# Performance work log

Measured on AMD Instinct MI355X. Metric: run time of the kernel, lower is better.

Reference implementation:

```python
import jax, jax.numpy as jnp
import numpy as np

B, N, H2, FD, P = 8, 128, 800, 500, 100


def setup_inputs() -> dict:
    key = jax.random.key(0)
    ks = jax.random.split(key, 20)
    w = lambda k, shape, s=0.05: jax.random.normal(k, shape, dtype=jnp.float32) * s
    return {
        "hidden_out": jax.random.normal(ks[0], (B, N, H2), dtype=jnp.float32),
        "Wh": w(ks[1], (FD, H2)), "bh": w(ks[2], (FD,)),
        "Wm": w(ks[3], (FD, H2)), "bm": w(ks[4], (FD,)),
        "Ws": w(ks[5], (FD, H2)), "bs": w(ks[6], (FD,)),
        "Wg": w(ks[7], (FD, H2)), "bg": w(ks[8], (FD,)),
        "W_gp": w(ks[9], (P, 3 * FD)), "b_gp": w(ks[10], (P,)),
        "W_sp": w(ks[11], (P, 3 * FD)), "b_sp": w(ks[12], (P,)),
        "W_rp": w(ks[13], (P, 2 * FD)), "b_rp": w(ks[14], (P,)),
        "w_go": w(ks[15], (1, P)), "b_go": w(ks[16], (1,)),
        "w_so": w(ks[17], (1, P)), "b_so": w(ks[18], (1,)),
    }


def reference(hidden_out, Wh, bh, Wm, bm, Ws, bs, Wg, bg,
              W_gp, b_gp, W_sp, b_sp, W_rp, b_rp,
              w_go, b_go, w_so, b_so):
    # hidden_out: [B, n, 2H]. Scores indexed [b, i(modifier), k(grand/sib), j(head)].
    n = hidden_out.shape[1]
    Fd = Wh.shape[0]
    # tanh(cat(...)) is elementwise, so tanh each per-position projection.
    head = jnp.tanh(jnp.einsum('bnh,fh->bnf', hidden_out, Wh) + bh)
    mod  = jnp.tanh(jnp.einsum('bnh,fh->bnf', hidden_out, Wm) + bm)
    sib  = jnp.tanh(jnp.einsum('bnh,fh->bnf', hidden_out, Ws) + bs)
    grd  = jnp.tanh(jnp.einsum('bnh,fh->bnf', hidden_out, Wg) + bg)

    # grand_out(grand_preout(x)) is a composed linear map (no nonlinearity between),
    # so the score decomposes into per-position scalars.
    vg, vgh, vgm = [(w_go @ W_gp[:, a * Fd:(a + 1) * Fd]).ravel() for a in range(3)]
    c_g = (b_gp @ w_go.ravel()) + b_go[0]
    gk = grd @ vg   # [B, n] grand position k
    gj = head @ vgh  # [B, n] head position j
    gi = mod @ vgm   # [B, n] modifier position i
    grand_val = jnp.tanh(gi[:, :, None, None] + gk[:, None, :, None]
                         + gj[:, None, None, :] + c_g)  # [B, i, k, j]

    vsh, vss, vsm = [(w_so @ W_sp[:, a * Fd:(a + 1) * Fd]).ravel() for a in range(3)]
    c_s = (b_sp @ w_so.ravel()) + b_so[0]
    sk = head @ vsh  # s-head at position k
    sj = sib @ vss   # sibling at position j
    si = mod @ vsm   # s-modifier at position i
    sib_val = jnp.tanh(si[:, :, None, None] + sk[:, None, :, None]
                       + sj[:, None, None, :] + c_s)

    idx = jnp.arange(n)
    i_ = idx[:, None, None]
    k_ = idx[None, :, None]
    j_ = idx[None, None, :]
    valid = (i_ != 0) & (i_ != j_) & (j_ != k_)  # main triple-index branch

    grand_scores = jnp.where(valid, grand_val, -jnp.inf)
    sibling_scores = jnp.where(valid, sib_val, jnp.float32(0.0))

    # root branch: j = k = 0, i != 0; uses root_preout then grand_out.
    r0 = head[:, 0] @ (w_go @ W_rp[:, :Fd]).ravel()        # [B]
    ri = mod @ (w_go @ W_rp[:, Fd:]).ravel()                # [B, n]
    root = jnp.tanh(r0[:, None] + ri + (b_rp @ w_go.ravel()) + b_go[0])
    grand_scores = grand_scores.at[:, 1:, 0, 0].set(root[:, 1:])

    return grand_scores, sibling_scores
```

## Files before the change

### kernel.cpp

```cpp
#include <hip/hip_runtime.h>
#include <math.h>

#define FD 500
#define H2 800
#define NB 8
#define NN 128
#define NR (NB*NN)
#define NC (4*FD)

#define NEG_HUGE (-1.0e30f)

__device__ __forceinline__ float fast_tanh(float x) {
    float e = __expf(2.0f * x);
    return 1.0f - 2.0f / (e + 1.0f);
}

__global__ void prep_kernel(const float* __restrict__ W_gp, const float* __restrict__ b_gp,
                            const float* __restrict__ W_sp, const float* __restrict__ b_sp,
                            const float* __restrict__ W_rp, const float* __restrict__ b_rp,
                            const float* __restrict__ w_go, const float* __restrict__ b_go,
                            const float* __restrict__ w_so, const float* __restrict__ b_so,
                            float* __restrict__ sel, float* __restrict__ consts) {
    int v = blockIdx.x;
    int f = threadIdx.x;
    const float* wvec; const float* mat; int cols; int off;
    if (v < 3)      { wvec = w_go; mat = W_gp; cols = 3*FD; off = v*FD; }
    else if (v < 6) { wvec = w_so; mat = W_sp; cols = 3*FD; off = (v-3)*FD; }
    else            { wvec = w_go; mat = W_rp; cols = 2*FD; off = (v-6)*FD; }
    if (f < FD) {
        float s = 0.f;
        #pragma unroll 4
        for (int p = 0; p < 100; ++p) s += wvec[p] * mat[p*cols + off + f];
        sel[v*512 + f] = s;
    }
    if (v == 0 && f >= FD && f < FD+3) {
        int which = f - FD;
        const float* bv; const float* wv; float badd;
        if (which == 0)      { bv = b_gp; wv = w_go; badd = b_go[0]; }
        else if (which == 1) { bv = b_sp; wv = w_so; badd = b_so[0]; }
        else                 { bv = b_rp; wv = w_go; badd = b_go[0]; }
        float s = badd;
        for (int p = 0; p < 100; ++p) s += bv[p] * wv[p];
        consts[which] = s;
    }
}

#define BM 64
#define BN 64
#define KT 16

__global__ __launch_bounds__(256) void gemm_tanh_kernel(
        const float* __restrict__ A,
        const float* __restrict__ Wh, const float* __restrict__ bh,
        const float* __restrict__ Wm, const float* __restrict__ bm,
        const float* __restrict__ Ws, const float* __restrict__ bs,
        const float* __restrict__ Wg, const float* __restrict__ bg,
        float* __restrict__ T) {
    __shared__ float As[KT][BM];
    __shared__ float Bs[KT][BN];
    int tid = threadIdx.x;
    int c0 = blockIdx.x * BN;
    int r0 = blockIdx.y * BM;

    int lm = tid & 63;
    int lk = tid >> 6;

    const float* arow = A + (size_t)(r0 + lm) * H2;

    int c = c0 + lm; if (c >= NC) c = NC - 1;
    int wt = c / FD, wf = c % FD;
    const float* wmat = (wt==0)?Wh:(wt==1)?Wm:(wt==2)?Ws:Wg;
    const float* wrow = wmat + (size_t)wf * H2;

    float acc[4][4];
    #pragma unroll
    for (int i=0;i<4;++i)
        #pragma unroll
        for (int j=0;j<4;++j) acc[i][j]=0.f;

    int tm = tid & 15;
    int tn = tid >> 4;

    float4 aReg = *(const float4*)(arow + lk*4);
    float4 wReg = *(const float4*)(wrow + lk*4);

    const int NT = H2 / KT;
    for (int kt = 0; kt < NT; ++kt) {
        __syncthreads();
        As[lk*4+0][lm] = aReg.x; As[lk*4+1][lm] = aReg.y;
        As[lk*4+2][lm] = aReg.z; As[lk*4+3][lm] = aReg.w;
        Bs[lk*4+0][lm] = wReg.x; Bs[lk*4+1][lm] = wReg.y;
        Bs[lk*4+2][lm] = wReg.z; Bs[lk*4+3][lm] = wReg.w;
        __syncthreads();
        if (kt+1 < NT) {
            aReg = *(const float4*)(arow + (kt+1)*KT + lk*4);
            wReg = *(const float4*)(wrow + (kt+1)*KT + lk*4);
        }
        #pragma unroll
        for (int k = 0; k < KT; ++k) {
            float4 a4 = *(const float4*)&As[k][tm*4];
            float4 b4 = *(const float4*)&Bs[k][tn*4];
            float av[4] = {a4.x,a4.y,a4.z,a4.w};
            float bv[4] = {b4.x,b4.y,b4.z,b4.w};
            #pragma unroll
            for (int i=0;i<4;++i)
                #pragma unroll
                for (int j=0;j<4;++j)
                    acc[i][j] += av[i]*bv[j];
        }
    }

    int cbase = c0 + tn*4;
    if (cbase < NC) {
        float bias[4];
        #pragma unroll
        for (int j=0;j<4;++j) {
            int cc = cbase + j;
            int t2 = cc / FD, f2 = cc % FD;
            const float* bb = (t2==0)?bh:(t2==1)?bm:(t2==2)?bs:bg;
            bias[j] = bb[f2];
        }
        #pragma unroll
        for (int i=0;i<4;++i) {
            int r = r0 + tm*4 + i;
            float4 o;
            o.x = fast_tanh(acc[i][0] + bias[0]);
            o.y = fast_tanh(acc[i][1] + bias[1]);
            o.z = fast_tanh(acc[i][2] + bias[2]);
            o.w = fast_tanh(acc[i][3] + bias[3]);
            *(float4*)(T + (size_t)r*NC + cbase) = o;
        }
    }
}

__global__ __launch_bounds__(256) void reduce_kernel(
        const float* __restrict__ T, const float* __restrict__ sel,
        float* __restrict__ rowvals) {
    int r = blockIdx.x;
    int tid = threadIdx.x;
    float p[8];
    #pragma unroll
    for (int q=0;q<8;++q) p[q]=0.f;
    const float* trow = T + (size_t)r * NC;
    for (int c = tid; c < NC; c += 256) {
        float y = trow[c];
        int t2 = c / FD, f2 = c % FD;
        if (t2 == 0) {
            p[1] += y * sel[1*512 + f2];
            p[5] += y * sel[3*512 + f2];
            p[7] += y * sel[6*512 + f2];
        } else if (t2 == 1) {
            p[0] += y * sel[2*512 + f2];
            p[3] += y * sel[5*512 + f2];
            p[6] += y * sel[7*512 + f2];
        } else if (t2 == 2) {
            p[4] += y * sel[4*512 + f2];
        } else {
            p[2] += y * sel[0*512 + f2];
        }
    }
    __shared__ float red[256][8];
    #pragma unroll
    for (int q=0;q<8;++q) red[tid][q] = p[q];
    __syncthreads();
    for (int s = 128; s > 0; s >>= 1) {
        if (tid < s) {
            #pragma unroll
            for (int q=0;q<8;++q) red[tid][q] += red[tid+s][q];
        }
        __syncthreads();
    }
    if (tid < 8) rowvals[(size_t)r*8 + tid] = red[0][tid];
}

#define KSPLIT 2
__global__ __launch_bounds__(256) void fill_kernel(
        const float* __restrict__ rowvals, const float* __restrict__ consts,
        float* __restrict__ grand, float* __restrict__ sib) {
    int bi = blockIdx.x;
    int kz = blockIdx.y;
    int b = bi >> 7;
    int i = bi & 127;
    int tid = threadIdx.x;

    __shared__ float gks[128], gjs[128], sks[128], sjs[128];
    if (tid < 128) {
        const float* rv = rowvals + (size_t)(b*128 + tid)*8;
        gks[tid] = rv[2];
        gjs[tid] = rv[1];
        sks[tid] = rv[5];
        sjs[tid] = rv[4];
    }
    __syncthreads();

    const float* rvi = rowvals + (size_t)bi * 8;
    float gi = rvi[0], si = rvi[3];
    float c_g = consts[0], c_s = consts[1], c_r = consts[2];
    float r0 = rowvals[(size_t)(b*128)*8 + 7];
    float ri = rvi[6];
    float rootv = fast_tanh(r0 + ri + c_r);

    size_t base = (size_t)bi * (128*128);

    int j4 = (tid & 31) * 4;
    int klo = tid >> 5;
    const int KROWS = 128 / KSPLIT;

    for (int it = 0; it < KROWS/8; ++it) {
        int k = kz*KROWS + it*8 + klo;
        float gk = gks[k], sk = sks[k];
        float4 go, so;
        #pragma unroll
        for (int jj = 0; jj < 4; ++jj) {
            int j = j4 + jj;
            bool valid = (i != 0) && (i != j) && (j != k);
            float g = valid ? fast_tanh(gi + gk + gjs[j] + c_g) : NEG_HUGE;
            float s = valid ? fast_tanh(si + sk + sjs[j] + c_s) : 0.0f;
            if (i != 0 && k == 0 && j == 0) g = rootv;
            (&go.x)[jj] = g;
            (&so.x)[jj] = s;
        }
        size_t off = base + (size_t)k*128 + j4;
        *(float4*)(grand + off) = go;
        *(float4*)(sib + off) = so;
    }
}

extern "C" void kernel_launch(void* const* d_in, const int* in_sizes, int n_in,
                              void* d_out, int out_size, void* d_ws, size_t ws_size,
                              hipStream_t stream) {
    const float* hidden = (const float*)d_in[0];
    const float* Wh  = (const float*)d_in[1];   const float* bh  = (const float*)d_in[2];
    const float* Wm  = (const float*)d_in[3];   const float* bm  = (const float*)d_in[4];
    const float* Ws_ = (const float*)d_in[5];   const float* bs  = (const float*)d_in[6];
    const float* Wg  = (const float*)d_in[7];   const float* bg  = (const float*)d_in[8];
    const float* W_gp = (const float*)d_in[9];  const float* b_gp = (const float*)d_in[10];
    const float* W_sp = (const float*)d_in[11]; const float* b_sp = (const float*)d_in[12];
    const float* W_rp = (const float*)d_in[13]; const float* b_rp = (const float*)d_in[14];
    const float* w_go = (const float*)d_in[15]; const float* b_go = (const float*)d_in[16];
    const float* w_so = (const float*)d_in[17]; const float* b_so = (const float*)d_in[18];

    float* out   = (float*)d_out;
    float* grand = out;
    float* sib   = out + (size_t)16777216;

    float* T       = (float*)d_ws;
    float* sel     = T + 2048000;
    float* consts  = sel + 4096;
    float* rowvals = consts + 16;

    prep_kernel<<<dim3(8), dim3(512), 0, stream>>>(W_gp, b_gp, W_sp, b_sp, W_rp, b_rp,
                                                   w_go, b_go, w_so, b_so, sel, consts);
    gemm_tanh_kernel<<<dim3(32,16), dim3(256), 0, stream>>>(hidden, Wh, bh, Wm, bm,
                                                            Ws_, bs, Wg, bg, T);
    reduce_kernel<<<dim3(NR), dim3(256), 0, stream>>>(T, sel, rowvals);
    fill_kernel<<<dim3(NR, KSPLIT), dim3(256), 0, stream>>>(rowvals, consts, grand, sib);
}
```

Baseline: 101.0 us.

## Use split-bf16 MFMA GEMM with fused tanh and projection reduction

Replaces the FP32 SIMT GEMM with a bf16x3 (hi/lo split) MFMA GEMM whose operands are pre-converted into a fragment-friendly tiled layout, staged through the output buffer as scratch. The tanh and the per-row dot products against the selector vectors are fused into the GEMM epilogue, which writes per-column-block partials instead of the full 1024x2000 activation matrix. A small finish kernel sums the partials. This removes the large intermediate write/read and the slow FP32 FMA loop, at the cost of extra convert passes and a small loss of precision from the split-bf16 emulation.

```diff
diff --git a/kernel.cpp b/kernel.cpp
--- a/kernel.cpp
+++ b/kernel.cpp
@@ -3,17 +3,23 @@
 
 #define FD 500
 #define H2 800
-#define NB 8
-#define NN 128
-#define NR (NB*NN)
-#define NC (4*FD)
+#define NRR 1024
+#define NPAD 2048
+#define NKS 25
 
 #define NEG_HUGE (-1.0e30f)
+
+typedef __bf16 bf16x8 __attribute__((ext_vector_type(8)));
+typedef float f32x4 __attribute__((ext_vector_type(4)));
+
+union ChunkU { uint4 u; bf16x8 b; __bf16 h[8]; };
 
 __device__ __forceinline__ float fast_tanh(float x) {
     float e = __expf(2.0f * x);
     return 1.0f - 2.0f / (e + 1.0f);
 }
+
+__device__ __forceinline__ bf16x8 as_frag(uint4 v) { ChunkU c; c.u = v; return c.b; }
 
 __global__ void prep_kernel(const float* __restrict__ W_gp, const float* __restrict__ b_gp,
                             const float* __restrict__ W_sp, const float* __restrict__ b_sp,
@@ -45,132 +51,176 @@
     }
 }
 
-#define BM 64
-#define BN 64
-#define KT 16
-
-__global__ __launch_bounds__(256) void gemm_tanh_kernel(
-        const float* __restrict__ A,
-        const float* __restrict__ Wh, const float* __restrict__ bh,
-        const float* __restrict__ Wm, const float* __restrict__ bm,
-        const float* __restrict__ Ws, const float* __restrict__ bs,
-        const float* __restrict__ Wg, const float* __restrict__ bg,
-        float* __restrict__ T) {
-    __shared__ float As[KT][BM];
-    __shared__ float Bs[KT][BN];
+__global__ void prep2_kernel(const float* __restrict__ sel,
+                             const float* __restrict__ bh, const float* __restrict__ bm,
+                             const float* __restrict__ bs, const float* __restrict__ bg,
+                             float* __restrict__ S8, float* __restrict__ bias_c) {
+    int c = blockIdx.x * 256 + threadIdx.x;
+    float v[8] = {0,0,0,0,0,0,0,0};
+    float bias = 0.f;
+    if (c < 2000) {
+        int t = c / FD, f = c % FD;
+        if (t == 0)      { v[1]=sel[1*512+f]; v[5]=sel[3*512+f]; v[7]=sel[6*512+f]; bias=bh[f]; }
+        else if (t == 1) { v[0]=sel[2*512+f]; v[3]=sel[5*512+f]; v[6]=sel[7*512+f]; bias=bm[f]; }
+        else if (t == 2) { v[4]=sel[4*512+f]; bias=bs[f]; }
+        else             { v[2]=sel[0*512+f]; bias=bg[f]; }
+    }
+    #pragma unroll
+    for (int q = 0; q < 8; ++q) S8[q*NPAD + c] = v[q];
+    bias_c[c] = bias;
+}
+
+__global__ __launch_bounds__(256) void convert_kernel(
+        const float* __restrict__ hidden,
+        const float* __restrict__ Wh, const float* __restrict__ Wm,
+        const float* __restrict__ Ws, const float* __restrict__ Wg,
+        uint4* __restrict__ A_t, uint4* __restrict__ B_t) {
+    int gid = blockIdx.x * 256 + threadIdx.x;
+    const float* src = nullptr;
+    uint4* dst;
+    int l, f;
+    if (gid < 102400) {
+        l = gid & 63; f = (gid >> 6) & 3;
+        int rest = gid >> 8;
+        int ks = rest % NKS, rb = rest / NKS;
+        int row = rb*64 + f*16 + (l & 15);
+        int k0 = ks*32 + (l >> 4)*8;
+        src = hidden + (size_t)row * H2 + k0;
+        dst = A_t + (size_t)(rb*NKS + ks) * 512;
+    } else {
+        int g2 = gid - 102400;
+        l = g2 & 63; f = (g2 >> 6) & 3;
+        int rest = g2 >> 8;
+        int ks = rest % NKS, cb = rest / NKS;
+        int c = cb*64 + f*16 + (l & 15);
+        int k0 = ks*32 + (l >> 4)*8;
+        if (c < 2000) {
+            int wt = c / FD, wf = c % FD;
+            const float* wm = (wt==0)?Wh:(wt==1)?Wm:(wt==2)?Ws:Wg;
+            src = wm + (size_t)wf * H2 + k0;
+        }
+        dst = B_t + (size_t)(cb*NKS + ks) * 512;
+    }
+    float x[8] = {0,0,0,0,0,0,0,0};
+    if (src) {
+        float4 v0 = *(const float4*)src;
+        float4 v1 = *(const float4*)(src + 4);
+        x[0]=v0.x; x[1]=v0.y; x[2]=v0.z; x[3]=v0.w;
+        x[4]=v1.x; x[5]=v1.y; x[6]=v1.z; x[7]=v1.w;
+    }
+    ChunkU hc, lo;
+    #pragma unroll
+    for (int j = 0; j < 8; ++j) {
+        __bf16 h = (__bf16)x[j];
+        hc.h[j] = h;
+        lo.h[j] = (__bf16)(x[j] - (float)h);
+    }
+    dst[(0*4 + f)*64 + l] = hc.u;
+    dst[(1*4 + f)*64 + l] = lo.u;
+}
+
+__global__ __launch_bounds__(256, 2) void gemm_kernel(
+        const uint4* __restrict__ A_t, const uint4* __restrict__ B_t,
+        const float* __restrict__ S8, const float* __restrict__ bias_c,
+        float* __restrict__ partials) {
+    __shared__ uint4 Abuf[2][512];
+    __shared__ uint4 Bbuf[2][512];
     int tid = threadIdx.x;
-    int c0 = blockIdx.x * BN;
-    int r0 = blockIdx.y * BM;
-
-    int lm = tid & 63;
-    int lk = tid >> 6;
-
-    const float* arow = A + (size_t)(r0 + lm) * H2;
-
-    int c = c0 + lm; if (c >= NC) c = NC - 1;
-    int wt = c / FD, wf = c % FD;
-    const float* wmat = (wt==0)?Wh:(wt==1)?Wm:(wt==2)?Ws:Wg;
-    const float* wrow = wmat + (size_t)wf * H2;
-
-    float acc[4][4];
-    #pragma unroll
-    for (int i=0;i<4;++i)
-        #pragma unroll
-        for (int j=0;j<4;++j) acc[i][j]=0.f;
-
-    int tm = tid & 15;
-    int tn = tid >> 4;
-
-    float4 aReg = *(const float4*)(arow + lk*4);
-    float4 wReg = *(const float4*)(wrow + lk*4);
-
-    const int NT = H2 / KT;
-    for (int kt = 0; kt < NT; ++kt) {
-        __syncthreads();
-        As[lk*4+0][lm] = aReg.x; As[lk*4+1][lm] = aReg.y;
-        As[lk*4+2][lm] = aReg.z; As[lk*4+3][lm] = aReg.w;
-        Bs[lk*4+0][lm] = wReg.x; Bs[lk*4+1][lm] = wReg.y;
-        Bs[lk*4+2][lm] = wReg.z; Bs[lk*4+3][lm] = wReg.w;
-        __syncthreads();
-        if (kt+1 < NT) {
-            aReg = *(const float4*)(arow + (kt+1)*KT + lk*4);
-            wReg = *(const float4*)(wrow + (kt+1)*KT + lk*4);
-        }
-        #pragma unroll
-        for (int k = 0; k < KT; ++k) {
-            float4 a4 = *(const float4*)&As[k][tm*4];
-            float4 b4 = *(const float4*)&Bs[k][tn*4];
-            float av[4] = {a4.x,a4.y,a4.z,a4.w};
-            float bv[4] = {b4.x,b4.y,b4.z,b4.w};
+    int cb = blockIdx.x;
+    int rb = blockIdx.y;
+    int l  = tid & 63;
+    int wid = tid >> 6;
+    int wr = wid >> 1, wc = wid & 1;
+
+    const uint4* Ablk = A_t + (size_t)rb * NKS * 512;
+    const uint4* Bblk = B_t + (size_t)cb * NKS * 512;
+
+    uint4 st[4];
+    #define STAGE_LOAD(ks) do { \
+        const uint4* s_ = (tid < 128) ? (Ablk + (ks)*512 + tid) : (Bblk + (ks)*512 + (tid-128)); \
+        st[0]=s_[0]; st[1]=s_[128]; st[2]=s_[256]; st[3]=s_[384]; } while(0)
+    #define STAGE_WRITE(buf) do { \
+        uint4* d_ = (tid < 128) ? &Abuf[buf][tid] : &Bbuf[buf][tid-128]; \
+        d_[0]=st[0]; d_[128]=st[1]; d_[256]=st[2]; d_[384]=st[3]; } while(0)
+
+    f32x4 acc[2][2];
+    #pragma unroll
+    for (int m=0;m<2;++m)
+        #pragma unroll
+        for (int n=0;n<2;++n) acc[m][n] = (f32x4){0.f,0.f,0.f,0.f};
+
+    STAGE_LOAD(0); STAGE_WRITE(0);
+    __syncthreads();
+    STAGE_LOAD(1);
+
+    for (int ks = 0; ks < NKS; ++ks) {
+        int cur = ks & 1;
+        int fa = wr*2, fb = wc*2;
+        bf16x8 a_h[2], a_l[2], b_h[2], b_l[2];
+        #pragma unroll
+        for (int m=0;m<2;++m) {
+            a_h[m] = as_frag(Abuf[cur][(0 + fa + m)*64 + l]);
+            a_l[m] = as_frag(Abuf[cur][(4 + fa + m)*64 + l]);
+        }
+        #pragma unroll
+        for (int n=0;n<2;++n) {
+            b_h[n] = as_frag(Bbuf[cur][(0 + fb + n)*64 + l]);
+            b_l[n] = as_frag(Bbuf[cur][(4 + fb + n)*64 + l]);
+        }
+        #pragma unroll
+        for (int m=0;m<2;++m)
             #pragma unroll
-            for (int i=0;i<4;++i)
-                #pragma unroll
-                for (int j=0;j<4;++j)
-                    acc[i][j] += av[i]*bv[j];
-        }
-    }
-
-    int cbase = c0 + tn*4;
-    if (cbase < NC) {
-        float bias[4];
-        #pragma unroll
-        for (int j=0;j<4;++j) {
-            int cc = cbase + j;
-            int t2 = cc / FD, f2 = cc % FD;
-            const float* bb = (t2==0)?bh:(t2==1)?bm:(t2==2)?bs:bg;
-            bias[j] = bb[f2];
-        }
-        #pragma unroll
-        for (int i=0;i<4;++i) {
-            int r = r0 + tm*4 + i;
-            float4 o;
-            o.x = fast_tanh(acc[i][0] + bias[0]);
-            o.y = fast_tanh(acc[i][1] + bias[1]);
-            o.z = fast_tanh(acc[i][2] + bias[2]);
-            o.w = fast_tanh(acc[i][3] + bias[3]);
-            *(float4*)(T + (size_t)r*NC + cbase) = o;
-        }
-    }
-}
-
-__global__ __launch_bounds__(256) void reduce_kernel(
-        const float* __restrict__ T, const float* __restrict__ sel,
-        float* __restrict__ rowvals) {
-    int r = blockIdx.x;
-    int tid = threadIdx.x;
-    float p[8];
-    #pragma unroll
-    for (int q=0;q<8;++q) p[q]=0.f;
-    const float* trow = T + (size_t)r * NC;
-    for (int c = tid; c < NC; c += 256) {
-        float y = trow[c];
-        int t2 = c / FD, f2 = c % FD;
-        if (t2 == 0) {
-            p[1] += y * sel[1*512 + f2];
-            p[5] += y * sel[3*512 + f2];
-            p[7] += y * sel[6*512 + f2];
-        } else if (t2 == 1) {
-            p[0] += y * sel[2*512 + f2];
-            p[3] += y * sel[5*512 + f2];
-            p[6] += y * sel[7*512 + f2];
-        } else if (t2 == 2) {
-            p[4] += y * sel[4*512 + f2];
-        } else {
-            p[2] += y * sel[0*512 + f2];
-        }
-    }
-    __shared__ float red[256][8];
-    #pragma unroll
-    for (int q=0;q<8;++q) red[tid][q] = p[q];
+            for (int n=0;n<2;++n) {
+                acc[m][n] = __builtin_amdgcn_mfma_f32_16x16x32_bf16(a_h[m], b_h[n], acc[m][n], 0,0,0);
+                acc[m][n] = __builtin_amdgcn_mfma_f32_16x16x32_bf16(a_h[m], b_l[n], acc[m][n], 0,0,0);
+                acc[m][n] = __builtin_amdgcn_mfma_f32_16x16x32_bf16(a_l[m], b_h[n], acc[m][n], 0,0,0);
+            }
+        if (ks + 1 < NKS) {
+            __syncthreads();
+            STAGE_WRITE((ks+1) & 1);
+            __syncthreads();
+            if (ks + 2 < NKS) STAGE_LOAD(ks+2);
+        }
+    }
+
+    int lr = l >> 4, lc = l & 15;
     __syncthreads();
-    for (int s = 128; s > 0; s >>= 1) {
-        if (tid < s) {
+    float* Y = (float*)Abuf;
+    #pragma unroll
+    for (int n=0;n<2;++n) {
+        int col_local = (wc*2 + n)*16 + lc;
+        float bias = bias_c[cb*64 + col_local];
+        #pragma unroll
+        for (int m=0;m<2;++m) {
+            int row_base = (wr*2 + m)*16 + lr*4;
             #pragma unroll
-            for (int q=0;q<8;++q) red[tid][q] += red[tid+s][q];
-        }
-        __syncthreads();
-    }
-    if (tid < 8) rowvals[(size_t)r*8 + tid] = red[0][tid];
+            for (int r=0;r<4;++r)
+                Y[(row_base + r)*64 + col_local] = fast_tanh(acc[m][n][r] + bias);
+        }
+    }
+    __syncthreads();
+    #pragma unroll
+    for (int it=0; it<2; ++it) {
+        int task = tid + it*256;
+        int q = task & 7, row = task >> 3;
+        const float* s8r = S8 + q*NPAD + cb*64;
+        const float* yr = Y + row*64;
+        float s = 0.f;
+        #pragma unroll 8
+        for (int c2=0;c2<64;++c2) s += yr[c2] * s8r[c2];
+        partials[((size_t)cb*NRR + rb*64 + row)*8 + q] = s;
+    }
+    #undef STAGE_LOAD
+    #undef STAGE_WRITE
+}
+
+__global__ void finish_kernel(const float* __restrict__ partials,
+                              float* __restrict__ rowvals) {
+    int t = blockIdx.x*256 + threadIdx.x;
+    float s = 0.f;
+    #pragma unroll 8
+    for (int cbk = 0; cbk < 32; ++cbk) s += partials[(size_t)cbk*8192 + t];
+    rowvals[t] = s;
 }
 
 #define KSPLIT 2
@@ -244,15 +294,21 @@
     float* grand = out;
     float* sib   = out + (size_t)16777216;
 
-    float* T       = (float*)d_ws;
-    float* sel     = T + 2048000;
+    uint4* A_t = (uint4*)out;
+    uint4* B_t = (uint4*)out + 204800;
+
+    float* S8      = (float*)d_ws;
+    float* bias_c  = S8 + 16384;
+    float* sel     = bias_c + 2048;
     float* consts  = sel + 4096;
     float* rowvals = consts + 16;
+    float* partials= rowvals + 8192;
 
     prep_kernel<<<dim3(8), dim3(512), 0, stream>>>(W_gp, b_gp, W_sp, b_sp, W_rp, b_rp,
                                                    w_go, b_go, w_so, b_so, sel, consts);
-    gemm_tanh_kernel<<<dim3(32,16), dim3(256), 0, stream>>>(hidden, Wh, bh, Wm, bm,
-                                                            Ws_, bs, Wg, bg, T);
-    reduce_kernel<<<dim3(NR), dim3(256), 0, stream>>>(T, sel, rowvals);
-    fill_kernel<<<dim3(NR, KSPLIT), dim3(256), 0, stream>>>(rowvals, consts, grand, sib);
-}
+    prep2_kernel<<<dim3(8), dim3(256), 0, stream>>>(sel, bh, bm, bs, bg, S8, bias_c);
+    convert_kernel<<<dim3(1200), dim3(256), 0, stream>>>(hidden, Wh, Wm, Ws_, Wg, A_t, B_t);
+    gemm_kernel<<<dim3(32,16), dim3(256), 0, stream>>>(A_t, B_t, S8, bias_c, partials);
+    finish_kernel<<<dim3(32), dim3(256), 0, stream>>>(partials, rowvals);
+    fill_kernel<<<dim3(1024, KSPLIT), dim3(256), 0, stream>>>(rowvals, consts, grand, sib);
+}
```

Measured after the change: 110.0 us. +8.9%, slower.
